# Kernel optimization log

Hardware: AMD Instinct MI355X
Metric: run time of the kernel (lower is better)

## Reference

```python
import jax, jax.numpy as jnp
import numpy as np

P = 8          # patch_num_in == patch_num_out
R = 16         # patch_resolution (pixels per patch side)
C = 2          # dim_channel
D = 512        # dim_token
NH = 8         # nhead
DFF = 2048     # dim_feedforward
L = 6          # num_layers
PAIRS = 5      # demo_num
BS = 8
HW = P * R     # 128
S = PAIRS * 2 * P * P  # 640 tokens
EPS = 1e-5


def _patchify(x):
    # x: (N, c, H, W) -> (N, P*P, c*R*R)
    N, c, H, W = x.shape
    x = x.reshape(N, c, P, R, P, R).transpose(0, 2, 4, 1, 3, 5)
    return x.reshape(N, P * P, c * R * R)


def _depatchify(x, c):
    # x: (N, P*P, c*R*R) -> (N, c, P*R, P*R)
    N = x.shape[0]
    x = x.reshape(N, P, P, c, R, R).transpose(0, 3, 1, 4, 2, 5)
    return x.reshape(N, c, P * R, P * R)


def _ln(x, s, b):
    mu = jnp.mean(x, axis=-1, keepdims=True)
    var = jnp.mean(jnp.square(x - mu), axis=-1, keepdims=True)
    return (x - mu) * jax.lax.rsqrt(var + EPS) * s + b


def _block_lowtri_additive_mask(seq_len):
    blk = jnp.arange(seq_len) // (P * P)  # alternating init/end blocks of size P*P
    allowed = blk[:, None] >= blk[None, :]
    return jnp.where(allowed, 0.0, -jnp.inf).astype(jnp.float32)


def setup_inputs() -> dict:
    key = jax.random.key(0)
    ks = jax.random.split(key, 20)
    s = 0.02
    f32 = jnp.float32
    inp = {
        "init": jax.random.normal(ks[0], (BS, PAIRS, C, HW, HW), f32),
        "end": jax.random.normal(ks[1], (BS, PAIRS, C, HW, HW), f32),
        "c_mask": jnp.ones((BS, C), dtype=bool),
        "pre_W": (jax.random.normal(ks[2], (D, C * R * R), f32) * s),
        "pre_b": jnp.zeros((D,), f32),
        "post_W": (jax.random.normal(ks[3], (C * R * R, D), f32) * s),
        "post_b": jnp.zeros((C * R * R,), f32),
        "patch_pos": jax.random.normal(ks[4], (P * P, D), f32),
        "func_pos": jax.random.normal(ks[5], (PAIRS * 2, D), f32),
        "Wqkv": (jax.random.normal(ks[6], (L, 3 * D, D), f32) * s),
        "bqkv": jnp.zeros((L, 3 * D), f32),
        "Wo": (jax.random.normal(ks[7], (L, D, D), f32) * s),
        "bo": jnp.zeros((L, D), f32),
        "ln1_s": jnp.ones((L, D), f32),
        "ln1_b": jnp.zeros((L, D), f32),
        "ln2_s": jnp.ones((L, D), f32),
        "ln2_b": jnp.zeros((L, D), f32),
        "W1": (jax.random.normal(ks[8], (L, DFF, D), f32) * s),
        "b1": jnp.zeros((L, DFF), f32),
        "W2": (jax.random.normal(ks[9], (L, D, DFF), f32) * s),
        "b2": jnp.zeros((L, D), f32),
    }
    return inp


def _forward(init, end, pre_W, pre_b, post_W, post_b, patch_pos, func_pos,
             Wqkv, bqkv, Wo, bo, ln1_s, ln1_b, ln2_s, ln2_b, W1, b1, W2, b2):
    bs, pairs = init.shape[0], init.shape[1]
    # interleave (init, end) per pair: (bs, pairs, 2, c, h, w)
    x = jnp.concatenate([init[:, :, None], end[:, :, None]], axis=2)
    f = x.reshape(-1, C, HW, HW)
    f = _patchify(f)                                    # (N, P*P, C*R*R)
    f = f @ pre_W.T + pre_b                             # (N, P*P, D)
    f = f + patch_pos                                   # patch pos encoding
    f = f.reshape(bs, pairs * 2, P * P, D)
    f = f + func_pos[: pairs * 2][None, :, None, :]     # func pos encoding
    seq = pairs * 2 * P * P
    f = f.reshape(bs, seq, D)

    amask = _block_lowtri_additive_mask(seq)            # (S, S) additive
    dh = D // NH
    scale = 1.0 / np.sqrt(dh).astype(np.float32)

    for l in range(L):
        qkv = f @ Wqkv[l].T + bqkv[l]                   # (bs, S, 3D)
        q, k, v = jnp.split(qkv, 3, axis=-1)
        q = q.reshape(bs, seq, NH, dh).transpose(0, 2, 1, 3)
        k = k.reshape(bs, seq, NH, dh).transpose(0, 2, 1, 3)
        v = v.reshape(bs, seq, NH, dh).transpose(0, 2, 1, 3)
        scores = jnp.einsum('bhqd,bhkd->bhqk', q, k) * scale + amask
        attn = jax.nn.softmax(scores, axis=-1)
        o = jnp.einsum('bhqk,bhkd->bhqd', attn, v)
        o = o.transpose(0, 2, 1, 3).reshape(bs, seq, D)
        o = o @ Wo[l].T + bo[l]
        f = _ln(f + o, ln1_s[l], ln1_b[l])              # post-norm (PyTorch default)
        ff = jax.nn.gelu(f @ W1[l].T + b1[l], approximate=False) @ W2[l].T + b2[l]
        f = _ln(f + ff, ln2_s[l], ln2_b[l])

    f = f.reshape(bs, pairs, 2, P * P, D)[:, :, 0]      # read prediction off init slots
    f = f @ post_W.T + post_b                           # (bs, pairs, P*P, C*R*R)
    f = f.reshape(bs * pairs, P * P, C * R * R)
    f = _depatchify(f, C)
    return f.reshape(bs, pairs, C, HW, HW)


def reference(init, end, c_mask, pre_W, pre_b, post_W, post_b, patch_pos, func_pos,
              Wqkv, bqkv, Wo, bo, ln1_s, ln1_b, ln2_s, ln2_b, W1, b1, W2, b2):
    # c_mask is unpacked but unused by the original forward
    return _forward(init, end, pre_W, pre_b, post_W, post_b, patch_pos, func_pos,
                    Wqkv, bqkv, Wo, bo, ln1_s, ln1_b, ln2_s, ln2_b, W1, b1, W2, b2)
```

## Files before the change

### kernel.cpp

```cpp
#include <hip/hip_runtime.h>
#include <hip/hip_bf16.h>

#define BSZ 8
#define PAIRS 5
#define NCH 2
#define HWP 128
#define PP 64
#define DIM 512
#define NHEAD 8
#define DHEAD 64
#define DFF 2048
#define NLAYER 6
#define SEQ 640
#define NTOK (BSZ * SEQ)
#define FIN 10
#define MPOST (BSZ * PAIRS * PP)

typedef unsigned short u16;
typedef __bf16 bf16_t;
typedef __attribute__((ext_vector_type(8))) __bf16 bf16x8;
typedef __attribute__((ext_vector_type(8))) unsigned short u16x8;
typedef __attribute__((ext_vector_type(4))) unsigned short u16x4;
typedef __attribute__((ext_vector_type(4))) float f32x4;
#define MFMA16(a, b, c) __builtin_amdgcn_mfma_f32_16x16x32_bf16(a, b, c, 0, 0, 0)

__device__ __forceinline__ u16 f2b(float x) {
  unsigned u = __float_as_uint(x);
  return (u16)((u + 0x7fffu + ((u >> 16) & 1u)) >> 16);
}

__device__ __forceinline__ float gelu_t(float x) {
  float y = 0.7978845608f * (x + 0.044715f * x * x * x);
  y = fminf(fmaxf(y, -10.f), 10.f);
  float e = __expf(2.f * y);
  return 0.5f * x * (1.f + (e - 1.f) / (e + 1.f));
}

__device__ __forceinline__ void dma16(const u16* g, void* l) {
  __builtin_amdgcn_global_load_lds(
      (const __attribute__((address_space(1))) void*)g,
      (__attribute__((address_space(3))) void*)l, 16, 0, 0);
}

template <int N> __device__ __forceinline__ void vwait() {
  if constexpr (N == 0) asm volatile("s_waitcnt vmcnt(0)" ::: "memory");
  else if constexpr (N == 2) asm volatile("s_waitcnt vmcnt(2)" ::: "memory");
  else if constexpr (N == 3) asm volatile("s_waitcnt vmcnt(3)" ::: "memory");
  else if constexpr (N == 4) asm volatile("s_waitcnt vmcnt(4)" ::: "memory");
  else if constexpr (N == 6) asm volatile("s_waitcnt vmcnt(6)" ::: "memory");
}

#define W_QKV (3 * DIM * DIM)
#define W_O (DIM * DIM)
#define W_1 (DFF * DIM)
#define OFF_O W_QKV
#define OFF_1 (W_QKV + W_O)
#define OFF_2 (W_QKV + W_O + W_1)
#define W_ALL (W_QKV + W_O + 2 * W_1)
#define PREPOST (2 * DIM * DIM)
#define N_CVT (PREPOST + NLAYER * W_ALL)

__global__ __launch_bounds__(256) void k_cvt_all(const float* __restrict__ preW,
                                                 const float* __restrict__ postW,
                                                 const float* __restrict__ wq,
                                                 const float* __restrict__ wo,
                                                 const float* __restrict__ w1,
                                                 const float* __restrict__ w2,
                                                 u16* __restrict__ dst) {
  size_t i = ((size_t)blockIdx.x * 256 + threadIdx.x) * 8;
  const float* src;
  size_t off;
  if (i < DIM * DIM) { src = preW; off = i; }
  else if (i < PREPOST) { src = postW; off = i - DIM * DIM; }
  else {
    size_t j = i - PREPOST;
    int l = (int)(j / W_ALL);
    size_t r = j - (size_t)l * W_ALL;
    if (r < OFF_O) { src = wq + (size_t)l * W_QKV; off = r; }
    else if (r < OFF_1) { src = wo + (size_t)l * W_O; off = r - OFF_O; }
    else if (r < OFF_2) { src = w1 + (size_t)l * W_1; off = r - OFF_1; }
    else { src = w2 + (size_t)l * W_1; off = r - OFF_2; }
  }
  float4 v0 = *(const float4*)(src + off);
  float4 v1 = *(const float4*)(src + off + 4);
  u16x8 o;
  o[0] = f2b(v0.x); o[1] = f2b(v0.y); o[2] = f2b(v0.z); o[3] = f2b(v0.w);
  o[4] = f2b(v1.x); o[5] = f2b(v1.y); o[6] = f2b(v1.z); o[7] = f2b(v1.w);
  *(u16x8*)(dst + i) = o;
}

__global__ __launch_bounds__(256) void k_patchify(const float* __restrict__ init,
                                                  const float* __restrict__ endp,
                                                  u16* __restrict__ A) {
  int i = blockIdx.x * 256 + threadIdx.x;
  int d = i & 511;
  int g = i >> 9;
  int p = g & 63;
  int fi = (g >> 6) % FIN;
  int b = g / SEQ;
  int e = fi & 1;
  int pr = fi >> 1;
  int c = d >> 8;
  int r1 = (d >> 4) & 15;
  int r2 = d & 15;
  int row = ((p >> 3) << 4) + r1;
  int col = ((p & 7) << 4) + r2;
  const float* src = e ? endp : init;
  size_t off = ((size_t)((b * PAIRS + pr) * NCH + c) << 14) + (size_t)row * HWP + col;
  A[i] = f2b(src[off]);
}

template <int BM, int NT, int MODE, int GATHER>
__global__ __launch_bounds__(256) void k_mma(const u16* __restrict__ A,
                                             const u16* __restrict__ B,
                                             const float* __restrict__ bias,
                                             u16* __restrict__ outB,
                                             float* __restrict__ outP,
                                             float* __restrict__ outF,
                                             const float* __restrict__ pp,
                                             const float* __restrict__ fp,
                                             int M, int N, int K, int act) {
  constexpr int FJ = NT / 32;
  constexpr int MI = BM / 32;
  constexpr int ACH = BM / 16;
  constexpr int NC = (BM / 16 + NT / 16) / 4;
  __shared__ __align__(16) bf16_t As[4][BM][32];
  __shared__ __align__(16) bf16_t Bs[4][NT][32];
  const int t = threadIdx.x;
  const int w = t >> 6, lane = t & 63, quad = lane >> 4, l16 = lane & 15;
  int bx = blockIdx.x, by = blockIdx.y;
  if ((gridDim.y & 7) == 0) {
    int lin = bx + gridDim.x * by;
    int xcd = lin & 7, slot = lin >> 3;
    int gx = gridDim.x;
    by = (gridDim.y >> 3) * xcd + slot / gx;
    bx = slot % gx;
  }
  const int row0 = by * BM, col0 = bx * NT;
  const int mB = (w & 1) * (BM / 2);
  const int nB = (w >> 1) * (NT / 2);

  const u16* aP[ACH];
#pragma unroll
  for (int c = 0; c < ACH; ++c) {
    int r = row0 + c * 16 + (lane >> 2);
    int g = r;
    if (GATHER) {
      int p = r & 63, pr = (r >> 6) % PAIRS, b = r / (PAIRS * PP);
      g = b * SEQ + pr * 128 + p;
    }
    aP[c] = A + (size_t)g * K + ((lane & 3) << 3);
  }
  const u16* bP = B + (size_t)(col0 + (lane >> 2)) * K + ((lane & 3) << 3);

  f32x4 acc[MI][FJ];
#pragma unroll
  for (int i = 0; i < MI; ++i)
#pragma unroll
    for (int j = 0; j < FJ; ++j) acc[i][j] = (f32x4){0.f, 0.f, 0.f, 0.f};

  auto stage = [&](int bu, int kk) {
#pragma unroll
    for (int s = 0; s < NC; ++s) {
      int c = NC * w + s;
      if (c < ACH) dma16(aP[c] + kk, &As[bu][c * 16][0]);
      else dma16(bP + (size_t)((c - ACH) * 16) * K + kk, &Bs[bu][(c - ACH) * 16][0]);
    }
  };

  const int iters = K >> 5;
  stage(0, 0);
  stage(1, 32);
  for (int it = 0; it < iters; ++it) {
    const int cur = it & 3;
    if (it + 2 < iters) stage((it + 2) & 3, (it + 2) << 5);
    if (it + 2 < iters) vwait<2 * NC>();
    else if (it + 1 < iters) vwait<NC>();
    else vwait<0>();
    asm volatile("s_barrier" ::: "memory");
    bf16x8 af[MI], bfr[FJ];
#pragma unroll
    for (int i = 0; i < MI; ++i)
      af[i] = *(const bf16x8*)&As[cur][mB + i * 16 + l16][quad * 8];
#pragma unroll
    for (int j = 0; j < FJ; ++j)
      bfr[j] = *(const bf16x8*)&Bs[cur][nB + j * 16 + l16][quad * 8];
#pragma unroll
    for (int i = 0; i < MI; ++i)
#pragma unroll
      for (int j = 0; j < FJ; ++j) acc[i][j] = MFMA16(af[i], bfr[j], acc[i][j]);
  }

#pragma unroll
  for (int i = 0; i < MI; ++i)
#pragma unroll
    for (int reg = 0; reg < 4; ++reg) {
      int m = row0 + mB + i * 16 + quad * 4 + reg;
#pragma unroll
      for (int j = 0; j < FJ; ++j) {
        int n = col0 + nB + j * 16 + l16;
        float v = acc[i][j][reg];
        if (MODE == 0) {
          v += bias[n];
          if (act) v = gelu_t(v);
          outB[(size_t)m * N + n] = f2b(v);
        } else if (MODE == 1) {
          outP[(size_t)m * N + n] = v;
        } else if (MODE == 2) {
          int p = m & 63, fi = (m >> 6) % FIN;
          v += bias[n] + pp[p * DIM + n] + fp[fi * DIM + n];
          outF[(size_t)m * N + n] = v;
          outB[(size_t)m * N + n] = f2b(v);
        } else {
          v += bias[n];
          int p = m & 63, pr = (m >> 6) % PAIRS, b = m / (PAIRS * PP);
          int c = n >> 8, r1 = (n >> 4) & 15, r2 = n & 15;
          int row = ((p >> 3) << 4) + r1, col = ((p & 7) << 4) + r2;
          size_t off = ((size_t)((b * PAIRS + pr) * NCH + c) << 14) +
                       (size_t)row * HWP + col;
          outF[off] = v;
        }
      }
    }
}

__global__ __launch_bounds__(256) void k_attn(const u16* __restrict__ qkv,
                                              u16* __restrict__ o, int qmul) {
  __shared__ bf16_t Qs[64][72];
  __shared__ bf16_t Ks[64][72];
  __shared__ bf16_t Vs[64][72];
  __shared__ bf16_t Ps[64][72];
  const int t = threadIdx.x;
  const int w = t >> 6, lane = t & 63, quad = lane >> 4, l16 = lane & 15;
  const int qblk = blockIdx.x * qmul, h = blockIdx.y, b = blockIdx.z;
  const int q0 = qblk << 6;
  const u16* base = qkv + (size_t)b * SEQ * (3 * DIM);
  const int sr = t >> 2;
  const int sd = (t & 3) << 4;
  const int rowB = 3 * DIM;
  {
    const u16* qp = base + (size_t)(q0 + sr) * rowB + h * DHEAD + sd;
    *(bf16x8*)&Qs[sr][sd] = *(const bf16x8*)(const void*)qp;
    *(bf16x8*)&Qs[sr][sd + 8] = *(const bf16x8*)(const void*)(qp + 8);
  }
  __syncthreads();
  bf16x8 aQ0 = *(const bf16x8*)&Qs[w * 16 + l16][quad * 8];
  bf16x8 aQ1 = *(const bf16x8*)&Qs[w * 16 + l16][32 + quad * 8];
  f32x4 accO[4];
#pragma unroll
  for (int j = 0; j < 4; ++j) accO[j] = (f32x4){0.f, 0.f, 0.f, 0.f};
  float mSt[4] = {-1e30f, -1e30f, -1e30f, -1e30f};
  float lSt[4] = {0.f, 0.f, 0.f, 0.f};
  const int ntile = qblk + 1;
  const u16* kp0 = base + (size_t)sr * rowB + DIM + h * DHEAD + sd;
  const u16* vp0 = base + (size_t)sr * rowB + 2 * DIM + h * DHEAD + sd;
  bf16x8 kR0 = *(const bf16x8*)(const void*)kp0;
  bf16x8 kR1 = *(const bf16x8*)(const void*)(kp0 + 8);
  bf16x8 vR0 = *(const bf16x8*)(const void*)vp0;
  bf16x8 vR1 = *(const bf16x8*)(const void*)(vp0 + 8);
  for (int kt = 0; kt < ntile; ++kt) {
    *(bf16x8*)&Ks[sr][sd] = kR0;
    *(bf16x8*)&Ks[sr][sd + 8] = kR1;
#pragma unroll
    for (int e = 0; e < 8; ++e) Vs[sd + e][sr] = vR0[e];
#pragma unroll
    for (int e = 0; e < 8; ++e) Vs[sd + 8 + e][sr] = vR1[e];
    if (kt + 1 < ntile) {
      const u16* kp = kp0 + (size_t)(kt + 1) * 64 * rowB;
      const u16* vp = vp0 + (size_t)(kt + 1) * 64 * rowB;
      kR0 = *(const bf16x8*)(const void*)kp;
      kR1 = *(const bf16x8*)(const void*)(kp + 8);
      vR0 = *(const bf16x8*)(const void*)vp;
      vR1 = *(const bf16x8*)(const void*)(vp + 8);
    }
    __syncthreads();
    f32x4 s[4];
#pragma unroll
    for (int j = 0; j < 4; ++j) {
      bf16x8 b0 = *(const bf16x8*)&Ks[j * 16 + l16][quad * 8];
      bf16x8 b1 = *(const bf16x8*)&Ks[j * 16 + l16][32 + quad * 8];
      s[j] = (f32x4){0.f, 0.f, 0.f, 0.f};
      s[j] = MFMA16(aQ0, b0, s[j]);
      s[j] = MFMA16(aQ1, b1, s[j]);
      s[j] *= 0.125f;
    }
#pragma unroll
    for (int reg = 0; reg < 4; ++reg) {
      float mx = fmaxf(fmaxf(s[0][reg], s[1][reg]), fmaxf(s[2][reg], s[3][reg]));
      mx = fmaxf(mx, __shfl_xor(mx, 1));
      mx = fmaxf(mx, __shfl_xor(mx, 2));
      mx = fmaxf(mx, __shfl_xor(mx, 4));
      mx = fmaxf(mx, __shfl_xor(mx, 8));
      float mNew = fmaxf(mSt[reg], mx);
      float alpha = __expf(mSt[reg] - mNew);
      mSt[reg] = mNew;
      float rs = 0.f;
#pragma unroll
      for (int j = 0; j < 4; ++j) {
        float p = __expf(s[j][reg] - mNew);
        s[j][reg] = p;
        rs += p;
      }
      rs += __shfl_xor(rs, 1);
      rs += __shfl_xor(rs, 2);
      rs += __shfl_xor(rs, 4);
      rs += __shfl_xor(rs, 8);
      lSt[reg] = lSt[reg] * alpha + rs;
#pragma unroll
      for (int j = 0; j < 4; ++j) accO[j][reg] *= alpha;
    }
#pragma unroll
    for (int j = 0; j < 4; ++j)
#pragma unroll
      for (int reg = 0; reg < 4; ++reg)
        *(u16*)&Ps[w * 16 + quad * 4 + reg][j * 16 + l16] = f2b(s[j][reg]);
    __syncthreads();
    bf16x8 aP0 = *(const bf16x8*)&Ps[w * 16 + l16][quad * 8];
    bf16x8 aP1 = *(const bf16x8*)&Ps[w * 16 + l16][32 + quad * 8];
#pragma unroll
    for (int jd = 0; jd < 4; ++jd) {
      bf16x8 b0 = *(const bf16x8*)&Vs[jd * 16 + l16][quad * 8];
      bf16x8 b1 = *(const bf16x8*)&Vs[jd * 16 + l16][32 + quad * 8];
      accO[jd] = MFMA16(aP0, b0, accO[jd]);
      accO[jd] = MFMA16(aP1, b1, accO[jd]);
    }
    __syncthreads();
  }
#pragma unroll
  for (int reg = 0; reg < 4; ++reg) {
    float inv = 1.0f / lSt[reg];
    int row = q0 + w * 16 + quad * 4 + reg;
#pragma unroll
    for (int jd = 0; jd < 4; ++jd)
      o[((size_t)(b * SEQ + row)) * DIM + h * DHEAD + jd * 16 + l16] =
          f2b(accO[jd][reg] * inv);
  }
}

template <int GIN>
__global__ __launch_bounds__(256) void k_red_ln(const float* __restrict__ part,
                                                const float* __restrict__ bias,
                                                const float* __restrict__ f_in,
                                                float* __restrict__ f_out,
                                                u16* __restrict__ fb_out,
                                                const float* __restrict__ s,
                                                const float* __restrict__ bvec) {
  const int t = threadIdx.x;
  const int half = t >> 7;
  const int r = blockIdx.x * 2 + half;
  const int c = (t & 127) * 4;
  int g = r;
  if (GIN) {
    int p = r & 63, pr = (r >> 6) % PAIRS, b = r / (PAIRS * PP);
    g = b * SEQ + pr * 128 + p;
  }
  float4 x = *(const float4*)(f_in + (size_t)g * DIM + c);
  float4 pa = *(const float4*)(part + (size_t)r * DIM + c);
  float4 bi = *(const float4*)(bias + c);
  x.x += pa.x + bi.x; x.y += pa.y + bi.y; x.z += pa.z + bi.z; x.w += pa.w + bi.w;
  float sum = x.x + x.y + x.z + x.w;
  float sq = x.x * x.x + x.y * x.y + x.z * x.z + x.w * x.w;
#pragma unroll
  for (int off = 32; off; off >>= 1) {
    sum += __shfl_xor(sum, off);
    sq += __shfl_xor(sq, off);
  }
  __shared__ float rs[4], rq[4];
  const int w = t >> 6, lane = t & 63;
  if (lane == 0) { rs[w] = sum; rq[w] = sq; }
  __syncthreads();
  float tot = rs[half * 2] + rs[half * 2 + 1];
  float tq2 = rq[half * 2] + rq[half * 2 + 1];
  float mu = tot * (1.0f / 512.0f);
  float var = tq2 * (1.0f / 512.0f) - mu * mu;
  float rstd = rsqrtf(var + 1e-5f);
  float4 sv = *(const float4*)(s + c);
  float4 bv = *(const float4*)(bvec + c);
  float4 o;
  o.x = (x.x - mu) * rstd * sv.x + bv.x;
  o.y = (x.y - mu) * rstd * sv.y + bv.y;
  o.z = (x.z - mu) * rstd * sv.z + bv.z;
  o.w = (x.w - mu) * rstd * sv.w + bv.w;
  *(float4*)(f_out + (size_t)r * DIM + c) = o;
  u16x4 ob;
  ob[0] = f2b(o.x); ob[1] = f2b(o.y); ob[2] = f2b(o.z); ob[3] = f2b(o.w);
  *(u16x4*)(fb_out + (size_t)r * DIM + c) = ob;
}

extern "C" void kernel_launch(void* const* d_in, const int* in_sizes, int n_in,
                              void* d_out, int out_size, void* d_ws, size_t ws_size,
                              hipStream_t stream) {
  const float* init = (const float*)d_in[0];
  const float* endp = (const float*)d_in[1];
  const float* pre_W = (const float*)d_in[3];
  const float* pre_b = (const float*)d_in[4];
  const float* post_W = (const float*)d_in[5];
  const float* post_b = (const float*)d_in[6];
  const float* patch_pos = (const float*)d_in[7];
  const float* func_pos = (const float*)d_in[8];
  const float* Wqkv = (const float*)d_in[9];
  const float* bqkv = (const float*)d_in[10];
  const float* Wo = (const float*)d_in[11];
  const float* bo = (const float*)d_in[12];
  const float* ln1_s = (const float*)d_in[13];
  const float* ln1_b = (const float*)d_in[14];
  const float* ln2_s = (const float*)d_in[15];
  const float* ln2_b = (const float*)d_in[16];
  const float* W1 = (const float*)d_in[17];
  const float* b1 = (const float*)d_in[18];
  const float* W2 = (const float*)d_in[19];
  const float* b2 = (const float*)d_in[20];
  float* out = (float*)d_out;

  char* p = (char*)d_ws;
  float* buf_f = (float*)p;    p += (size_t)NTOK * DIM * 4;
  u16* buf_fb = (u16*)p;       p += (size_t)NTOK * DIM * 2;
  u16* buf_attn = (u16*)p;     p += (size_t)NTOK * DIM * 2;
  u16* shared_b = (u16*)p;     p += (size_t)NTOK * DFF * 2;
  u16* wAll = (u16*)p;         p += (size_t)N_CVT * 2;
  float* partial = (float*)p;  p += (size_t)NTOK * DIM * 4;
  float* buf_fc = (float*)p;   p += (size_t)MPOST * DIM * 4;
  u16* buf_fbc = (u16*)p;      p += (size_t)MPOST * DIM * 2;
  u16* buf_patch = shared_b;
  u16* buf_qkv = shared_b;
  u16* buf_hid = shared_b;
  u16* wPre = wAll;
  u16* wPost = wAll + DIM * DIM;
  u16* wL = wAll + PREPOST;

  dim3 blk(256);
  const int elems = NTOK * DIM;

  k_cvt_all<<<N_CVT / (256 * 8), blk, 0, stream>>>(pre_W, post_W, Wqkv, Wo, W1, W2,
                                                   wAll);
  k_patchify<<<elems / 256, blk, 0, stream>>>(init, endp, buf_patch);
  k_mma<64, 64, 2, 0><<<dim3(8, 80), blk, 0, stream>>>(
      buf_patch, wPre, pre_b, buf_fb, nullptr, buf_f, patch_pos, func_pos,
      NTOK, DIM, DIM, 0);

  for (int l = 0; l < NLAYER; ++l) {
    u16* wB = wL + (size_t)l * W_ALL;
    k_mma<64, 64, 0, 0><<<dim3(24, 80), blk, 0, stream>>>(
        buf_fb, wB, bqkv + (size_t)l * 3 * DIM, buf_qkv, nullptr, nullptr, nullptr,
        nullptr, NTOK, 3 * DIM, DIM, 0);
    if (l < NLAYER - 1) {
      k_attn<<<dim3(SEQ / 64, NHEAD, BSZ), blk, 0, stream>>>(buf_qkv, buf_attn, 1);
      k_mma<64, 64, 1, 0><<<dim3(8, 80), blk, 0, stream>>>(
          buf_attn, wB + OFF_O, nullptr, nullptr, partial, nullptr, nullptr, nullptr,
          NTOK, DIM, DIM, 0);
      k_red_ln<0><<<NTOK / 2, blk, 0, stream>>>(partial, bo + (size_t)l * DIM,
                                                buf_f, buf_f, buf_fb,
                                                ln1_s + (size_t)l * DIM,
                                                ln1_b + (size_t)l * DIM);
      k_mma<64, 64, 0, 0><<<dim3(32, 80), blk, 0, stream>>>(
          buf_fb, wB + OFF_1, b1 + (size_t)l * DFF, buf_hid, nullptr, nullptr,
          nullptr, nullptr, NTOK, DFF, DIM, 1);
      k_mma<64, 64, 1, 0><<<dim3(8, 80), blk, 0, stream>>>(
          buf_hid, wB + OFF_2, nullptr, nullptr, partial, nullptr, nullptr, nullptr,
          NTOK, DIM, DFF, 0);
      k_red_ln<0><<<NTOK / 2, blk, 0, stream>>>(partial, b2 + (size_t)l * DIM,
                                                buf_f, buf_f, buf_fb,
                                                ln2_s + (size_t)l * DIM,
                                                ln2_b + (size_t)l * DIM);
    } else {
      k_attn<<<dim3(SEQ / 128, NHEAD, BSZ), blk, 0, stream>>>(buf_qkv, buf_attn, 2);
      k_mma<64, 64, 1, 1><<<dim3(8, 40), blk, 0, stream>>>(
          buf_attn, wB + OFF_O, nullptr, nullptr, partial, nullptr, nullptr, nullptr,
          MPOST, DIM, DIM, 0);
      k_red_ln<1><<<MPOST / 2, blk, 0, stream>>>(partial, bo + (size_t)l * DIM,
                                                 buf_f, buf_fc, buf_fbc,
                                                 ln1_s + (size_t)l * DIM,
                                                 ln1_b + (size_t)l * DIM);
      k_mma<64, 64, 0, 0><<<dim3(32, 40), blk, 0, stream>>>(
          buf_fbc, wB + OFF_1, b1 + (size_t)l * DFF, buf_hid, nullptr, nullptr,
          nullptr, nullptr, MPOST, DFF, DIM, 1);
      k_mma<64, 64, 1, 0><<<dim3(8, 40), blk, 0, stream>>>(
          buf_hid, wB + OFF_2, nullptr, nullptr, partial, nullptr, nullptr, nullptr,
          MPOST, DIM, DFF, 0);
      k_red_ln<0><<<MPOST / 2, blk, 0, stream>>>(partial, b2 + (size_t)l * DIM,
                                                 buf_fc, buf_fc, buf_fbc,
                                                 ln2_s + (size_t)l * DIM,
                                                 ln2_b + (size_t)l * DIM);
    }
  }

  k_mma<64, 64, 3, 0><<<dim3(8, 40), blk, 0, stream>>>(
      buf_fbc, wPost, post_b, nullptr, nullptr, out, nullptr, nullptr,
      MPOST, DIM, DIM, 0);
}
```

Measured before the change: 890.8 us.

## Double GEMM K-step to 64 and XOR-swizzle LDS tiles

The GEMM kernel now stages 64-wide K slices per pipeline step instead of 32, halving the number of barrier/wait iterations. The LDS rows are 128 bytes, and an XOR swizzle on the 16-byte chunk index is applied both in the global-to-LDS DMA addressing and in the fragment reads to avoid bank conflicts. This doubles LDS usage per buffer (4 stages), which may reduce occupancy, and it issues twice as many DMA loads per stage.

```diff
diff --git a/kernel.cpp b/kernel.cpp
--- a/kernel.cpp
+++ b/kernel.cpp
@@ -48,6 +48,7 @@
   else if constexpr (N == 3) asm volatile("s_waitcnt vmcnt(3)" ::: "memory");
   else if constexpr (N == 4) asm volatile("s_waitcnt vmcnt(4)" ::: "memory");
   else if constexpr (N == 6) asm volatile("s_waitcnt vmcnt(6)" ::: "memory");
+  else if constexpr (N == 8) asm volatile("s_waitcnt vmcnt(8)" ::: "memory");
 }
 
 #define W_QKV (3 * DIM * DIM)
@@ -122,10 +123,11 @@
                                              int M, int N, int K, int act) {
   constexpr int FJ = NT / 32;
   constexpr int MI = BM / 32;
-  constexpr int ACH = BM / 16;
-  constexpr int NC = (BM / 16 + NT / 16) / 4;
-  __shared__ __align__(16) bf16_t As[4][BM][32];
-  __shared__ __align__(16) bf16_t Bs[4][NT][32];
+  constexpr int ACH = BM / 8;
+  constexpr int BCH = NT / 8;
+  constexpr int NC = (ACH + BCH) / 4;
+  __shared__ __align__(16) bf16_t As[4][BM][64];
+  __shared__ __align__(16) bf16_t Bs[4][NT][64];
   const int t = threadIdx.x;
   const int w = t >> 6, lane = t & 63, quad = lane >> 4, l16 = lane & 15;
   int bx = blockIdx.x, by = blockIdx.y;
@@ -140,18 +142,20 @@
   const int mB = (w & 1) * (BM / 2);
   const int nB = (w >> 1) * (NT / 2);
 
+  const int lrow = lane >> 3;
+  const int lcol = (((lane & 7) ^ (lrow & 7)) << 3);
   const u16* aP[ACH];
 #pragma unroll
   for (int c = 0; c < ACH; ++c) {
-    int r = row0 + c * 16 + (lane >> 2);
+    int r = row0 + c * 8 + lrow;
     int g = r;
     if (GATHER) {
       int p = r & 63, pr = (r >> 6) % PAIRS, b = r / (PAIRS * PP);
       g = b * SEQ + pr * 128 + p;
     }
-    aP[c] = A + (size_t)g * K + ((lane & 3) << 3);
-  }
-  const u16* bP = B + (size_t)(col0 + (lane >> 2)) * K + ((lane & 3) << 3);
+    aP[c] = A + (size_t)g * K + lcol;
+  }
+  const u16* bP = B + (size_t)(col0 + lrow) * K + lcol;
 
   f32x4 acc[MI][FJ];
 #pragma unroll
@@ -163,32 +167,46 @@
 #pragma unroll
     for (int s = 0; s < NC; ++s) {
       int c = NC * w + s;
-      if (c < ACH) dma16(aP[c] + kk, &As[bu][c * 16][0]);
-      else dma16(bP + (size_t)((c - ACH) * 16) * K + kk, &Bs[bu][(c - ACH) * 16][0]);
+      if (c < ACH) dma16(aP[c] + kk, &As[bu][c * 8][0]);
+      else dma16(bP + (size_t)((c - ACH) * 8) * K + kk, &Bs[bu][(c - ACH) * 8][0]);
     }
   };
 
-  const int iters = K >> 5;
+  const int iters = K >> 6;
   stage(0, 0);
-  stage(1, 32);
+  stage(1, 64);
   for (int it = 0; it < iters; ++it) {
     const int cur = it & 3;
-    if (it + 2 < iters) stage((it + 2) & 3, (it + 2) << 5);
+    if (it + 2 < iters) stage((it + 2) & 3, (it + 2) << 6);
     if (it + 2 < iters) vwait<2 * NC>();
     else if (it + 1 < iters) vwait<NC>();
     else vwait<0>();
     asm volatile("s_barrier" ::: "memory");
-    bf16x8 af[MI], bfr[FJ];
-#pragma unroll
-    for (int i = 0; i < MI; ++i)
-      af[i] = *(const bf16x8*)&As[cur][mB + i * 16 + l16][quad * 8];
-#pragma unroll
-    for (int j = 0; j < FJ; ++j)
-      bfr[j] = *(const bf16x8*)&Bs[cur][nB + j * 16 + l16][quad * 8];
-#pragma unroll
-    for (int i = 0; i < MI; ++i)
-#pragma unroll
-      for (int j = 0; j < FJ; ++j) acc[i][j] = MFMA16(af[i], bfr[j], acc[i][j]);
+    const char* aB = (const char*)&As[cur][0][0];
+    const char* bB = (const char*)&Bs[cur][0][0];
+    bf16x8 af[2][MI], bfr[2][FJ];
+#pragma unroll
+    for (int h = 0; h < 2; ++h) {
+#pragma unroll
+      for (int i = 0; i < MI; ++i) {
+        int row = mB + i * 16 + l16;
+        af[h][i] = *(const bf16x8*)(aB + row * 128 +
+                                    (((quad + 4 * h) ^ (l16 & 7)) << 4));
+      }
+#pragma unroll
+      for (int j = 0; j < FJ; ++j) {
+        int row = nB + j * 16 + l16;
+        bfr[h][j] = *(const bf16x8*)(bB + row * 128 +
+                                     (((quad + 4 * h) ^ (l16 & 7)) << 4));
+      }
+    }
+#pragma unroll
+    for (int h = 0; h < 2; ++h)
+#pragma unroll
+      for (int i = 0; i < MI; ++i)
+#pragma unroll
+        for (int j = 0; j < FJ; ++j)
+          acc[i][j] = MFMA16(af[h][i], bfr[h][j], acc[i][j]);
   }
 
 #pragma unroll
```

Result: slower. 956.4 us (+7.4%).
